# Kernel tuning notes

Hardware: AMD Instinct MI355X
Metric: run time of the kernel (lower is better)

The kernel has to match this reference:

```python
import jax, jax.numpy as jnp
import numpy as np

B, N, HID, H, DH, NB = 4, 4096, 768, 12, 64, 266
EPS = 1e-4


def softmax_kernel(data, proj, is_query):
    # data: [B,H,N,DH], proj: [NB,DH]. FAVOR+ positive softmax features.
    d = data.shape[-1]
    ratio = proj.shape[0] ** -0.5
    dn = d ** -0.25  # data normalizer
    data_dash = jnp.einsum('bhnd,jd->bhnj', data * dn, proj)  # [B,H,N,NB]
    diag = 0.5 * jnp.sum((data * dn) ** 2, axis=-1, keepdims=True)  # [B,H,N,1]
    if is_query:
        m = jnp.max(data_dash, axis=-1, keepdims=True)
    else:
        m = jnp.max(data_dash, axis=(-1, -2), keepdims=True)
    return ratio * (jnp.exp(data_dash - diag - m) + EPS)


def setup_inputs() -> dict:
    key = jax.random.key(0)
    ks = jax.random.split(key, 8)
    s = HID ** -0.5
    return {
        'hidden_states': jax.random.normal(ks[0], (B, N, HID), jnp.float32),
        'Wq': jax.random.normal(ks[1], (HID, HID), jnp.float32) * s,
        'bq': jnp.zeros((HID,), jnp.float32),
        'Wk': jax.random.normal(ks[2], (HID, HID), jnp.float32) * s,
        'bk': jnp.zeros((HID,), jnp.float32),
        'Wv': jax.random.normal(ks[3], (HID, HID), jnp.float32) * s,
        'bv': jnp.zeros((HID,), jnp.float32),
        'proj': jax.random.normal(ks[4], (NB, DH), jnp.float32),
    }


def reference(hidden_states, Wq, bq, Wk, bk, Wv, bv, proj):
    def heads(x):  # [B,N,HID] -> [B,H,N,DH]
        return x.reshape(B, N, H, DH).transpose(0, 2, 1, 3)

    q = heads(hidden_states @ Wq.T + bq)
    k = heads(hidden_states @ Wk.T + bk)
    v = heads(hidden_states @ Wv.T + bv)

    qp = softmax_kernel(q, proj, True)   # [B,H,N,NB]
    kp = softmax_kernel(k, proj, False)  # [B,H,N,NB]

    # non-causal linear attention: out = q' (k'^T v) / (q' sum_n k')
    k_sum = jnp.sum(kp, axis=2)                               # [B,H,NB]
    d_inv = 1.0 / jnp.einsum('bhnj,bhj->bhn', qp, k_sum)      # [B,H,N]
    ctx = jnp.einsum('bhnj,bhnd->bhjd', kp, v)                # [B,H,NB,DH]
    out = jnp.einsum('bhnj,bhjd->bhnd', qp, ctx) * d_inv[..., None]

    return out.transpose(0, 2, 1, 3).reshape(B, N, HID)
```

## Files before the change

kernel.cpp:

```cpp
#include <hip/hip_runtime.h>
#include <hip/hip_bf16.h>
#include <stdint.h>

#define B_   4
#define N_   4096
#define HID_ 768
#define H_   12
#define DH_  64
#define NB_  266
#define NBP_ 288
#define EPS_ 1e-4f
#define RATIO_ 0.06131393f

typedef unsigned short u16;
typedef __attribute__((ext_vector_type(8))) short short8;
typedef __attribute__((ext_vector_type(4))) float floatx4;

__device__ __forceinline__ u16 f2b(float f) {
  __hip_bfloat16 h = __float2bfloat16(f);
  return *reinterpret_cast<u16*>(&h);
}
__device__ __forceinline__ float b2f(u16 u) {
  union { unsigned u; float f; } x; x.u = ((unsigned)u) << 16; return x.f;
}
__device__ __forceinline__ unsigned fmap(float x) {
  unsigned u = __float_as_uint(x);
  return (u & 0x80000000u) ? ~u : (u | 0x80000000u);
}
__device__ __forceinline__ float funmap(unsigned u) {
  unsigned b = (u & 0x80000000u) ? (u & 0x7FFFFFFFu) : ~u;
  return __uint_as_float(b);
}
__device__ __forceinline__ void gl16(const u16* g, u16* l) {
  __builtin_amdgcn_global_load_lds(
      (const __attribute__((address_space(1))) void*)g,
      (__attribute__((address_space(3))) void*)l, 16, 0, 0);
}

__global__ __launch_bounds__(256) void k_prep(
    const float4* __restrict__ hs, const float4* __restrict__ Wq,
    const float4* __restrict__ Wk, const float4* __restrict__ Wv,
    const float* __restrict__ proj,
    uint2* __restrict__ hsb, uint2* __restrict__ wb3, u16* __restrict__ projb,
    float4* __restrict__ zf, unsigned* __restrict__ mbuf) {
  int blk = blockIdx.x;
  const int t = threadIdx.x;
  if (blk < 12288) {
    int i = blk * 256 + t;
    float4 v = hs[i];
    union { u16 s[4]; uint2 u; } pk;
    pk.s[0] = f2b(v.x); pk.s[1] = f2b(v.y); pk.s[2] = f2b(v.z); pk.s[3] = f2b(v.w);
    hsb[i] = pk.u;
    return;
  }
  blk -= 12288;
  if (blk < 1728) {
    int i = blk * 256 + t;
    int sel = i / 147456, j = i - sel * 147456;
    const float4* s = (sel == 0) ? Wq : (sel == 1) ? Wk : Wv;
    float4 v = s[j];
    union { u16 s4[4]; uint2 u; } pk;
    pk.s4[0] = f2b(v.x); pk.s4[1] = f2b(v.y); pk.s4[2] = f2b(v.z); pk.s4[3] = f2b(v.w);
    wb3[i] = pk.u;
    return;
  }
  blk -= 1728;
  if (blk < 72) {
    int i = blk * 256 + t;
    int j = i / DH_, d = i - j * DH_;
    float v = (j < NB_) ? proj[j * DH_ + d] * 0.35355339059327373f : 0.f;
    projb[i] = f2b(v);
    return;
  }
  blk -= 72;
  if (blk < 878) {
    int i = blk * 256 + t;
    if (i < 224640) zf[i] = (float4){0.f, 0.f, 0.f, 0.f};
    return;
  }
  if (t < B_ * H_) mbuf[t] = 0u;
}

__global__ __launch_bounds__(256) void k_qkv(
    const u16* __restrict__ hsb, const u16* __restrict__ wb,
    const float* __restrict__ bq, const float* __restrict__ bk, const float* __restrict__ bv,
    u16* __restrict__ qb, u16* __restrict__ kb, u16* __restrict__ vT) {
  __shared__ u16 At[2 * 128 * 32];
  __shared__ u16 Bt[2 * 128 * 32];
  const int m0 = blockIdx.x * 128;
  const int bn = blockIdx.y;
  const int sel = bn / 6;
  const int or0 = (bn % 6) * 128;
  const u16* W = wb + (size_t)sel * HID_ * HID_;
  const int t = threadIdx.x, lane = t & 63, wv = t >> 6;
  const int wr = (wv >> 1) * 64, wc = (wv & 1) * 64;
  const int lm = lane & 15, lq = lane >> 4;
  const int srow = wv * 32 + (lane >> 2);
  const int scol = (lane & 3) * 8;
  const u16* gA = hsb + (size_t)(m0 + srow) * HID_ + scol;
  const u16* gB = W + (size_t)(or0 + srow) * HID_ + scol;
  u16* lA = At + wv * 1024;
  u16* lB = Bt + wv * 1024;
  floatx4 acc[4][4];
#pragma unroll
  for (int i = 0; i < 4; i++)
#pragma unroll
    for (int j = 0; j < 4; j++) acc[i][j] = (floatx4){0.f, 0.f, 0.f, 0.f};

  for (int k0 = 0; k0 < HID_; k0 += 64) {
    __syncthreads();
#pragma unroll
    for (int p = 0; p < 2; p++) {
#pragma unroll
      for (int i = 0; i < 2; i++) {
        gl16(gA + k0 + p * 32 + i * 16 * HID_, lA + p * 4096 + i * 512);
        gl16(gB + k0 + p * 32 + i * 16 * HID_, lB + p * 4096 + i * 512);
      }
    }
    __syncthreads();
#pragma unroll
    for (int p = 0; p < 2; p++) {
      short8 af[4], bfr[4];
#pragma unroll
      for (int mt = 0; mt < 4; mt++) af[mt] = *(const short8*)&At[p * 4096 + (wr + mt * 16 + lm) * 32 + lq * 8];
#pragma unroll
      for (int nt = 0; nt < 4; nt++) bfr[nt] = *(const short8*)&Bt[p * 4096 + (wc + nt * 16 + lm) * 32 + lq * 8];
#pragma unroll
      for (int mt = 0; mt < 4; mt++)
#pragma unroll
        for (int nt = 0; nt < 4; nt++)
          acc[mt][nt] = __builtin_amdgcn_mfma_f32_16x16x32_bf16(af[mt], bfr[nt], acc[mt][nt], 0, 0, 0);
    }
  }
  if (sel < 2) {
    const float* bias = (sel == 0) ? bq : bk;
    u16* dst = (sel == 0) ? qb : kb;
#pragma unroll
    for (int mt = 0; mt < 4; mt++) {
#pragma unroll
      for (int nt = 0; nt < 4; nt++) {
        int lc = or0 + wc + nt * 16 + lm;
        float bb = bias[lc];
#pragma unroll
        for (int r = 0; r < 4; r++) {
          int row = m0 + wr + mt * 16 + lq * 4 + r;
          dst[(size_t)row * HID_ + lc] = f2b(acc[mt][nt][r] + bb);
        }
      }
    }
  } else {
#pragma unroll
    for (int mt = 0; mt < 4; mt++) {
#pragma unroll
      for (int nt = 0; nt < 4; nt++) {
        int lc = or0 + wc + nt * 16 + lm;
        int hh = lc >> 6, dv = lc & 63;
        float bb = bv[lc];
        int rowbase = m0 + wr + mt * 16 + lq * 4;
        int b = rowbase >> 12, n = rowbase & 4095;
        union { u16 s[4]; uint2 u; } pk;
#pragma unroll
        for (int r = 0; r < 4; r++) pk.s[r] = f2b(acc[mt][nt][r] + bb);
        *(uint2*)(vT + ((size_t)(b * H_ + hh) * DH_ + dv) * N_ + n) = pk.u;
      }
    }
  }
}

__global__ __launch_bounds__(256) void k_kmax2(
    const u16* __restrict__ kb, const u16* __restrict__ projb, unsigned* __restrict__ mbuf) {
  const int bh = blockIdx.y, b = bh / H_, h = bh - b * H_;
  const int n0 = blockIdx.x * 256;
  const int t = threadIdx.x, lane = t & 63, wv = t >> 6;
  const int lm = lane & 15, lq = lane >> 4;
  const u16* kbase = kb + (size_t)(b * N_ + n0 + wv * 64) * HID_ + h * DH_;
  short8 af0[4], af1[4];
#pragma unroll
  for (int mt = 0; mt < 4; mt++) {
    const u16* p = kbase + (size_t)(mt * 16 + lm) * HID_ + lq * 8;
    af0[mt] = *(const short8*)p;
    af1[mt] = *(const short8*)(p + 32);
  }
  float mx = -3e38f;
  for (int ct = 0; ct < 17; ct++) {
    const u16* pp = projb + (ct * 16 + lm) * DH_ + lq * 8;
    short8 bf0 = *(const short8*)pp;
    short8 bf1 = *(const short8*)(pp + 32);
    bool valid = (ct < 16) || (lm < 10);
#pragma unroll
    for (int mt = 0; mt < 4; mt++) {
      floatx4 a = __builtin_amdgcn_mfma_f32_16x16x32_bf16(af0[mt], bf0, (floatx4){0.f,0.f,0.f,0.f}, 0, 0, 0);
      a = __builtin_amdgcn_mfma_f32_16x16x32_bf16(af1[mt], bf1, a, 0, 0, 0);
      if (valid) {
#pragma unroll
        for (int r = 0; r < 4; r++) mx = fmaxf(mx, a[r]);
      }
    }
  }
#pragma unroll
  for (int o = 1; o < 64; o <<= 1) mx = fmaxf(mx, __shfl_xor(mx, o));
  if (lane == 0) atomicMax(&mbuf[bh], fmap(mx));
}

__global__ __launch_bounds__(256) void k_ctx3(
    const u16* __restrict__ kb, const u16* __restrict__ vT, const u16* __restrict__ projb,
    const unsigned* __restrict__ mbuf, float* __restrict__ ctxTf, float* __restrict__ ksum) {
  __shared__ u16 kpl[NBP_ * 72];
  const int bh = blockIdx.y, b = bh / H_, h = bh - b * H_;
  const int n0 = blockIdx.x * 256;
  const int t = threadIdx.x, lane = t & 63, wv = t >> 6;
  const int lm = lane & 15, lq = lane >> 4;
  const float m = funmap(mbuf[bh]);
  const u16* vTb = vT + ((size_t)bh * DH_ + wv * 16 + lm) * N_;
  floatx4 acc[18];
#pragma unroll
  for (int jt = 0; jt < 18; jt++) acc[jt] = (floatx4){0.f, 0.f, 0.f, 0.f};
  float kacc[17];
#pragma unroll
  for (int ct = 0; ct < 17; ct++) kacc[ct] = 0.f;

  for (int it = 0; it < 4; it++) {
    const int n64 = n0 + it * 64;
    __syncthreads();
    {
      const int row = n64 + wv * 16 + lm;
      const u16* kr = kb + ((size_t)(b * N_) + row) * HID_ + h * DH_ + lq * 8;
      short8 af0 = *(const short8*)kr;
      short8 af1 = *(const short8*)(kr + 32);
      float rs = 0.f;
#pragma unroll
      for (int i = 0; i < 8; i++) { float f = b2f(((const u16*)&af0)[i]); rs += f * f; }
#pragma unroll
      for (int i = 0; i < 8; i++) { float f = b2f(((const u16*)&af1)[i]); rs += f * f; }
      rs += __shfl_xor(rs, 16);
      rs += __shfl_xor(rs, 32);
      float dg[4];
#pragma unroll
      for (int r = 0; r < 4; r++) dg[r] = 0.0625f * __shfl(rs, lq * 4 + r);
#pragma unroll
      for (int ct = 0; ct < 17; ct++) {
        const u16* pp = projb + (ct * 16 + lm) * DH_ + lq * 8;
        short8 bf0 = *(const short8*)pp;
        short8 bf1 = *(const short8*)(pp + 32);
        floatx4 a = __builtin_amdgcn_mfma_f32_16x16x32_bf16(af0, bf0, (floatx4){0.f,0.f,0.f,0.f}, 0, 0, 0);
        a = __builtin_amdgcn_mfma_f32_16x16x32_bf16(af1, bf1, a, 0, 0, 0);
        bool valid = (ct < 16) || (lm < 10);
        union { u16 s[4]; uint2 u; } pk;
        float kss = 0.f;
#pragma unroll
        for (int r = 0; r < 4; r++) {
          float val = valid ? RATIO_ * (__expf(a[r] - dg[r] - m) + EPS_) : 0.f;
          kss += val;
          pk.s[r] = f2b(val);
        }
        kacc[ct] += kss;
        *(uint2*)&kpl[(ct * 16 + lm) * 72 + wv * 16 + lq * 4] = pk.u;
      }
      *(uint2*)&kpl[(272 + lm) * 72 + wv * 16 + lq * 4] = make_uint2(0u, 0u);
    }
    __syncthreads();
#pragma unroll
    for (int ns = 0; ns < 2; ns++) {
      short8 av = *(const short8*)(vTb + n64 + ns * 32 + lq * 8);
#pragma unroll
      for (int jt = 0; jt < 18; jt++) {
        short8 bf = *(const short8*)&kpl[(jt * 16 + lm) * 72 + ns * 32 + lq * 8];
        acc[jt] = __builtin_amdgcn_mfma_f32_16x16x32_bf16(av, bf, acc[jt], 0, 0, 0);
      }
    }
  }
#pragma unroll
  for (int ct = 0; ct < 17; ct++) {
    float v = kacc[ct];
    v += __shfl_xor(v, 16);
    v += __shfl_xor(v, 32);
    if (lq == 0) atomicAdd(&ksum[bh * NBP_ + ct * 16 + lm], v);
  }
#pragma unroll
  for (int jt = 0; jt < 18; jt++) {
#pragma unroll
    for (int r = 0; r < 4; r++)
      atomicAdd(&ctxTf[((size_t)bh * DH_ + wv * 16 + lq * 4 + r) * NBP_ + jt * 16 + lm], acc[jt][r]);
  }
}

__global__ void k_cvt_ctx(const float* __restrict__ src, u16* __restrict__ dst) {
  int i = blockIdx.x * 256 + threadIdx.x;
  if (i < B_ * H_ * DH_ * NBP_) dst[i] = f2b(src[i]);
}

__global__ __launch_bounds__(256) void k_out3(
    const u16* __restrict__ qb, const u16* __restrict__ projb,
    const u16* __restrict__ ctxb, const float* __restrict__ ksum,
    float* __restrict__ outp) {
  __shared__ u16 qpl[4][16][296];
  const int bh = blockIdx.y, b = bh / H_, h = bh - b * H_;
  const int n0 = blockIdx.x * 256;
  const int t = threadIdx.x, lane = t & 63, wv = t >> 6;
  const int lm = lane & 15, lq = lane >> 4;
  const u16* qbase = qb + (size_t)(b * N_ + n0 + wv * 64) * HID_ + h * DH_;
  const u16* cb = ctxb + (size_t)bh * DH_ * NBP_;
  const float* ksb = ksum + bh * NBP_;
  float ksv[17];
#pragma unroll
  for (int ct = 0; ct < 17; ct++) ksv[ct] = ksb[ct * 16 + lm];

  for (int mt = 0; mt < 4; mt++) {
    const u16* prow = qbase + (size_t)(mt * 16 + lm) * HID_ + lq * 8;
    short8 af0 = *(const short8*)prow;
    short8 af1 = *(const short8*)(prow + 32);
    float rs = 0.f;
#pragma unroll
    for (int i = 0; i < 8; i++) { float f = b2f(((const u16*)&af0)[i]); rs += f * f; }
#pragma unroll
    for (int i = 0; i < 8; i++) { float f = b2f(((const u16*)&af1)[i]); rs += f * f; }
    rs += __shfl_xor(rs, 16);
    rs += __shfl_xor(rs, 32);
    float dg[4];
#pragma unroll
    for (int r = 0; r < 4; r++) dg[r] = 0.0625f * __shfl(rs, lq * 4 + r);

    float rm[4] = {-3e38f, -3e38f, -3e38f, -3e38f};
#pragma unroll
    for (int ct = 0; ct < 17; ct++) {
      const u16* pp = projb + (ct * 16 + lm) * DH_ + lq * 8;
      short8 bf0 = *(const short8*)pp;
      short8 bf1 = *(const short8*)(pp + 32);
      floatx4 a = __builtin_amdgcn_mfma_f32_16x16x32_bf16(af0, bf0, (floatx4){0.f,0.f,0.f,0.f}, 0, 0, 0);
      a = __builtin_amdgcn_mfma_f32_16x16x32_bf16(af1, bf1, a, 0, 0, 0);
      if ((ct < 16) || (lm < 10)) {
#pragma unroll
        for (int r = 0; r < 4; r++) rm[r] = fmaxf(rm[r], a[r]);
      }
    }
#pragma unroll
    for (int o = 1; o < 16; o <<= 1) {
#pragma unroll
      for (int r = 0; r < 4; r++) rm[r] = fmaxf(rm[r], __shfl_xor(rm[r], o));
    }
    float dpart[4] = {0.f, 0.f, 0.f, 0.f};
#pragma unroll
    for (int ct = 0; ct < 18; ct++) {
      floatx4 a;
      if (ct < 17) {
        const u16* pp = projb + (ct * 16 + lm) * DH_ + lq * 8;
        short8 bf0 = *(const short8*)pp;
        short8 bf1 = *(const short8*)(pp + 32);
        a = __builtin_amdgcn_mfma_f32_16x16x32_bf16(af0, bf0, (floatx4){0.f,0.f,0.f,0.f}, 0, 0, 0);
        a = __builtin_amdgcn_mfma_f32_16x16x32_bf16(af1, bf1, a, 0, 0, 0);
      } else {
        a = (floatx4){0.f, 0.f, 0.f, 0.f};
      }
      bool valid = (ct < 16) || (ct == 16 && lm < 10);
      float kv = (ct < 17) ? ksv[ct] : 0.f;
#pragma unroll
      for (int r = 0; r < 4; r++) {
        float qpv = valid ? RATIO_ * (__expf(a[r] - dg[r] - rm[r]) + EPS_) : 0.f;
        dpart[r] += qpv * kv;
        qpl[wv][lq * 4 + r][ct * 16 + lm] = f2b(qpv);
      }
    }
#pragma unroll
    for (int o = 1; o < 16; o <<= 1) {
#pragma unroll
      for (int r = 0; r < 4; r++) dpart[r] += __shfl_xor(dpart[r], o);
    }
    float dinv[4];
#pragma unroll
    for (int r = 0; r < 4; r++) dinv[r] = 1.f / dpart[r];

    floatx4 ao[4];
#pragma unroll
    for (int dt = 0; dt < 4; dt++) ao[dt] = (floatx4){0.f, 0.f, 0.f, 0.f};
#pragma unroll
    for (int ks9 = 0; ks9 < 9; ks9++) {
      short8 aq = *(const short8*)&qpl[wv][lm][ks9 * 32 + lq * 8];
#pragma unroll
      for (int dt = 0; dt < 4; dt++) {
        short8 bc = *(const short8*)(cb + (size_t)(dt * 16 + lm) * NBP_ + ks9 * 32 + lq * 8);
        ao[dt] = __builtin_amdgcn_mfma_f32_16x16x32_bf16(aq, bc, ao[dt], 0, 0, 0);
      }
    }
#pragma unroll
    for (int dt = 0; dt < 4; dt++) {
#pragma unroll
      for (int r = 0; r < 4; r++) {
        int n = n0 + wv * 64 + mt * 16 + lq * 4 + r;
        outp[((size_t)(b * N_ + n)) * HID_ + h * DH_ + dt * 16 + lm] = ao[dt][r] * dinv[r];
      }
    }
  }
}

extern "C" void kernel_launch(void* const* d_in, const int* in_sizes, int n_in,
                              void* d_out, int out_size, void* d_ws, size_t ws_size,
                              hipStream_t stream) {
  (void)in_sizes; (void)n_in; (void)out_size; (void)ws_size;
  const float* hs   = (const float*)d_in[0];
  const float* Wq   = (const float*)d_in[1];
  const float* bq   = (const float*)d_in[2];
  const float* Wk   = (const float*)d_in[3];
  const float* bk   = (const float*)d_in[4];
  const float* Wv   = (const float*)d_in[5];
  const float* bv   = (const float*)d_in[6];
  const float* proj = (const float*)d_in[7];

  char* w = (char*)d_ws;
  u16* hsb   = (u16*)w;  w += (size_t)16384 * 768 * 2;
  u16* wb3   = (u16*)w;  w += (size_t)3 * 768 * 768 * 2;
  u16* projb = (u16*)w;  w += (size_t)NBP_ * 64 * 2;
  u16* qb    = (u16*)w;  w += (size_t)16384 * 768 * 2;
  u16* kb    = (u16*)w;  w += (size_t)16384 * 768 * 2;
  u16* vT    = (u16*)w;  w += (size_t)48 * DH_ * N_ * 2;
  float* ksum  = (float*)w; w += (size_t)48 * NBP_ * 4;
  float* ctxTf = (float*)w; w += (size_t)48 * DH_ * NBP_ * 4;
  u16* ctxTb = (u16*)w;  w += (size_t)48 * DH_ * NBP_ * 2;
  unsigned* mbuf = (unsigned*)w;

  hipLaunchKernelGGL(k_prep, dim3(14967), dim3(256), 0, stream,
                     (const float4*)hs, (const float4*)Wq, (const float4*)Wk, (const float4*)Wv,
                     proj, (uint2*)hsb, (uint2*)wb3, projb, (float4*)ksum, mbuf);
  hipLaunchKernelGGL(k_qkv, dim3(128, 18), dim3(256), 0, stream, hsb, wb3, bq, bk, bv, qb, kb, vT);
  hipLaunchKernelGGL(k_kmax2, dim3(16, 48), dim3(256), 0, stream, kb, projb, mbuf);
  hipLaunchKernelGGL(k_ctx3, dim3(16, 48), dim3(256), 0, stream, kb, vT, projb, mbuf, ctxTf, ksum);
  hipLaunchKernelGGL(k_cvt_ctx, dim3((48 * DH_ * NBP_ + 255) / 256), dim3(256), 0, stream, ctxTf, ctxTb);
  hipLaunchKernelGGL(k_out3, dim3(16, 48), dim3(256), 0, stream, qb, projb, ctxTb, ksum, (float*)d_out);
}
```

Measured before the change: 405.7 us.

## Split ctx kernel over feature columns to drop atomics, zeroing and conversion pass

The context kernel is repartitioned so each block owns 32 random-feature columns of one head and loops over all 4096 tokens, instead of owning a token chunk and atomically accumulating the full 288x64 context. Blocks now write ksum and the bf16 context directly, which removes the zero-fill in the prep kernel, the float atomics and the separate conversion kernel. The key squared norms are computed once in the max kernel and stored for reuse, and the next token tile is prefetched. In exchange, each block recomputes the key features for its column slice over the whole sequence and re-reads the keys and values 9 times. The grid shrinks to 432 longer-running blocks, with a block-index swizzle over heads.

```diff
diff --git a/kernel.cpp b/kernel.cpp
--- a/kernel.cpp
+++ b/kernel.cpp
@@ -42,7 +42,7 @@
     const float4* __restrict__ Wk, const float4* __restrict__ Wv,
     const float* __restrict__ proj,
     uint2* __restrict__ hsb, uint2* __restrict__ wb3, u16* __restrict__ projb,
-    float4* __restrict__ zf, unsigned* __restrict__ mbuf) {
+    unsigned* __restrict__ mbuf) {
   int blk = blockIdx.x;
   const int t = threadIdx.x;
   if (blk < 12288) {
@@ -73,12 +73,7 @@
     return;
   }
   blk -= 72;
-  if (blk < 878) {
-    int i = blk * 256 + t;
-    if (i < 224640) zf[i] = (float4){0.f, 0.f, 0.f, 0.f};
-    return;
-  }
-  if (t < B_ * H_) mbuf[t] = 0u;
+  if (blk == 0 && t < B_ * H_) mbuf[t] = 0u;
 }
 
 __global__ __launch_bounds__(256) void k_qkv(
@@ -167,8 +162,9 @@
   }
 }
 
-__global__ __launch_bounds__(256) void k_kmax2(
-    const u16* __restrict__ kb, const u16* __restrict__ projb, unsigned* __restrict__ mbuf) {
+__global__ __launch_bounds__(256) void k_kmax3(
+    const u16* __restrict__ kb, const u16* __restrict__ projb,
+    unsigned* __restrict__ mbuf, float* __restrict__ diagk) {
   const int bh = blockIdx.y, b = bh / H_, h = bh - b * H_;
   const int n0 = blockIdx.x * 256;
   const int t = threadIdx.x, lane = t & 63, wv = t >> 6;
@@ -181,6 +177,17 @@
     af0[mt] = *(const short8*)p;
     af1[mt] = *(const short8*)(p + 32);
   }
+#pragma unroll
+  for (int mt = 0; mt < 4; mt++) {
+    float rs = 0.f;
+#pragma unroll
+    for (int i = 0; i < 8; i++) { float f = b2f(((const u16*)&af0[mt])[i]); rs += f * f; }
+#pragma unroll
+    for (int i = 0; i < 8; i++) { float f = b2f(((const u16*)&af1[mt])[i]); rs += f * f; }
+    rs += __shfl_xor(rs, 16);
+    rs += __shfl_xor(rs, 32);
+    if (lq == 0) diagk[(size_t)bh * N_ + n0 + wv * 64 + mt * 16 + lm] = 0.0625f * rs;
+  }
   float mx = -3e38f;
   for (int ct = 0; ct < 17; ct++) {
     const u16* pp = projb + (ct * 16 + lm) * DH_ + lq * 8;
@@ -202,91 +209,107 @@
   if (lane == 0) atomicMax(&mbuf[bh], fmap(mx));
 }
 
-__global__ __launch_bounds__(256) void k_ctx3(
+__global__ __launch_bounds__(256) void k_ctx4(
     const u16* __restrict__ kb, const u16* __restrict__ vT, const u16* __restrict__ projb,
-    const unsigned* __restrict__ mbuf, float* __restrict__ ctxTf, float* __restrict__ ksum) {
-  __shared__ u16 kpl[NBP_ * 72];
-  const int bh = blockIdx.y, b = bh / H_, h = bh - b * H_;
-  const int n0 = blockIdx.x * 256;
+    const unsigned* __restrict__ mbuf, const float* __restrict__ diagk,
+    float* __restrict__ ksum, u16* __restrict__ ctxb) {
+  __shared__ u16 kpl[32 * 72];
+  __shared__ float kred[4][2][16];
+  const int orig = blockIdx.x;
+  const int lg = (orig & 7) * 54 + (orig >> 3);
+  const int bh = lg / 9, jb = lg - bh * 9;
+  const int j0 = jb * 32;
+  const int b = bh / H_, h = bh - b * H_;
   const int t = threadIdx.x, lane = t & 63, wv = t >> 6;
   const int lm = lane & 15, lq = lane >> 4;
   const float m = funmap(mbuf[bh]);
+  const bool vj0 = (j0 + lm) < NB_;
+  const bool vj1 = (j0 + 16 + lm) < NB_;
+  short8 bp00, bp01, bp10, bp11;
+  {
+    const u16* pp = projb + (j0 + lm) * DH_ + lq * 8;
+    bp00 = *(const short8*)pp;
+    bp01 = *(const short8*)(pp + 32);
+    pp += 16 * DH_;
+    bp10 = *(const short8*)pp;
+    bp11 = *(const short8*)(pp + 32);
+  }
+  const u16* kbB = kb + (size_t)(b * N_) * HID_ + h * DH_;
   const u16* vTb = vT + ((size_t)bh * DH_ + wv * 16 + lm) * N_;
-  floatx4 acc[18];
-#pragma unroll
-  for (int jt = 0; jt < 18; jt++) acc[jt] = (floatx4){0.f, 0.f, 0.f, 0.f};
-  float kacc[17];
-#pragma unroll
-  for (int ct = 0; ct < 17; ct++) kacc[ct] = 0.f;
-
-  for (int it = 0; it < 4; it++) {
-    const int n64 = n0 + it * 64;
+  const float* dgB = diagk + (size_t)bh * N_;
+  floatx4 acc0 = (floatx4){0.f,0.f,0.f,0.f}, acc1 = (floatx4){0.f,0.f,0.f,0.f};
+  float kacc0 = 0.f, kacc1 = 0.f;
+  const u16* kr0 = kbB + (size_t)(wv * 16 + lm) * HID_ + lq * 8;
+  short8 af0 = *(const short8*)kr0;
+  short8 af1 = *(const short8*)(kr0 + 32);
+  floatx4 dg4 = *(const floatx4*)(dgB + wv * 16 + lq * 4);
+
+  for (int n64 = 0; n64 < N_; n64 += 64) {
+    __syncthreads();
+    const int nn = (n64 + 64 < N_) ? n64 + 64 : 0;
+    const u16* krn = kbB + (size_t)(nn + wv * 16 + lm) * HID_ + lq * 8;
+    short8 nf0 = *(const short8*)krn;
+    short8 nf1 = *(const short8*)(krn + 32);
+    floatx4 nd = *(const floatx4*)(dgB + nn + wv * 16 + lq * 4);
+    short8 av0 = *(const short8*)(vTb + n64 + lq * 8);
+    short8 av1 = *(const short8*)(vTb + n64 + 32 + lq * 8);
+    {
+      floatx4 a = __builtin_amdgcn_mfma_f32_16x16x32_bf16(af0, bp00, (floatx4){0.f,0.f,0.f,0.f}, 0, 0, 0);
+      a = __builtin_amdgcn_mfma_f32_16x16x32_bf16(af1, bp01, a, 0, 0, 0);
+      union { u16 s[4]; uint2 u; } pk;
+      float kss = 0.f;
+#pragma unroll
+      for (int r = 0; r < 4; r++) {
+        float val = vj0 ? RATIO_ * (__expf(a[r] - dg4[r] - m) + EPS_) : 0.f;
+        kss += val;
+        pk.s[r] = f2b(val);
+      }
+      kacc0 += kss;
+      *(uint2*)&kpl[lm * 72 + wv * 16 + lq * 4] = pk.u;
+      a = __builtin_amdgcn_mfma_f32_16x16x32_bf16(af0, bp10, (floatx4){0.f,0.f,0.f,0.f}, 0, 0, 0);
+      a = __builtin_amdgcn_mfma_f32_16x16x32_bf16(af1, bp11, a, 0, 0, 0);
+      kss = 0.f;
+#pragma unroll
+      for (int r = 0; r < 4; r++) {
+        float val = vj1 ? RATIO_ * (__expf(a[r] - dg4[r] - m) + EPS_) : 0.f;
+        kss += val;
+        pk.s[r] = f2b(val);
+      }
+      kacc1 += kss;
+      *(uint2*)&kpl[(16 + lm) * 72 + wv * 16 + lq * 4] = pk.u;
+    }
     __syncthreads();
     {
-      const int row = n64 + wv * 16 + lm;
-      const u16* kr = kb + ((size_t)(b * N_) + row) * HID_ + h * DH_ + lq * 8;
-      short8 af0 = *(const short8*)kr;
-      short8 af1 = *(const short8*)(kr + 32);
-      float rs = 0.f;
-#pragma unroll
-      for (int i = 0; i < 8; i++) { float f = b2f(((const u16*)&af0)[i]); rs += f * f; }
-#pragma unroll
-      for (int i = 0; i < 8; i++) { float f = b2f(((const u16*)&af1)[i]); rs += f * f; }
-      rs += __shfl_xor(rs, 16);
-      rs += __shfl_xor(rs, 32);
-      float dg[4];
-#pragma unroll
-      for (int r = 0; r < 4; r++) dg[r] = 0.0625f * __shfl(rs, lq * 4 + r);
-#pragma unroll
-      for (int ct = 0; ct < 17; ct++) {
-        const u16* pp = projb + (ct * 16 + lm) * DH_ + lq * 8;
-        short8 bf0 = *(const short8*)pp;
-        short8 bf1 = *(const short8*)(pp + 32);
-        floatx4 a = __builtin_amdgcn_mfma_f32_16x16x32_bf16(af0, bf0, (floatx4){0.f,0.f,0.f,0.f}, 0, 0, 0);
-        a = __builtin_amdgcn_mfma_f32_16x16x32_bf16(af1, bf1, a, 0, 0, 0);
-        bool valid = (ct < 16) || (lm < 10);
-        union { u16 s[4]; uint2 u; } pk;
-        float kss = 0.f;
-#pragma unroll
-        for (int r = 0; r < 4; r++) {
-          float val = valid ? RATIO_ * (__expf(a[r] - dg[r] - m) + EPS_) : 0.f;
-          kss += val;
-          pk.s[r] = f2b(val);
-        }
-        kacc[ct] += kss;
-        *(uint2*)&kpl[(ct * 16 + lm) * 72 + wv * 16 + lq * 4] = pk.u;
-      }
-      *(uint2*)&kpl[(272 + lm) * 72 + wv * 16 + lq * 4] = make_uint2(0u, 0u);
-    }
-    __syncthreads();
-#pragma unroll
-    for (int ns = 0; ns < 2; ns++) {
-      short8 av = *(const short8*)(vTb + n64 + ns * 32 + lq * 8);
-#pragma unroll
-      for (int jt = 0; jt < 18; jt++) {
-        short8 bf = *(const short8*)&kpl[(jt * 16 + lm) * 72 + ns * 32 + lq * 8];
-        acc[jt] = __builtin_amdgcn_mfma_f32_16x16x32_bf16(av, bf, acc[jt], 0, 0, 0);
-      }
-    }
-  }
-#pragma unroll
-  for (int ct = 0; ct < 17; ct++) {
-    float v = kacc[ct];
-    v += __shfl_xor(v, 16);
-    v += __shfl_xor(v, 32);
-    if (lq == 0) atomicAdd(&ksum[bh * NBP_ + ct * 16 + lm], v);
-  }
-#pragma unroll
-  for (int jt = 0; jt < 18; jt++) {
-#pragma unroll
-    for (int r = 0; r < 4; r++)
-      atomicAdd(&ctxTf[((size_t)bh * DH_ + wv * 16 + lq * 4 + r) * NBP_ + jt * 16 + lm], acc[jt][r]);
-  }
-}
-
-__global__ void k_cvt_ctx(const float* __restrict__ src, u16* __restrict__ dst) {
-  int i = blockIdx.x * 256 + threadIdx.x;
-  if (i < B_ * H_ * DH_ * NBP_) dst[i] = f2b(src[i]);
+      short8 bf = *(const short8*)&kpl[lm * 72 + lq * 8];
+      acc0 = __builtin_amdgcn_mfma_f32_16x16x32_bf16(av0, bf, acc0, 0, 0, 0);
+      bf = *(const short8*)&kpl[(16 + lm) * 72 + lq * 8];
+      acc1 = __builtin_amdgcn_mfma_f32_16x16x32_bf16(av0, bf, acc1, 0, 0, 0);
+      bf = *(const short8*)&kpl[lm * 72 + 32 + lq * 8];
+      acc0 = __builtin_amdgcn_mfma_f32_16x16x32_bf16(av1, bf, acc0, 0, 0, 0);
+      bf = *(const short8*)&kpl[(16 + lm) * 72 + 32 + lq * 8];
+      acc1 = __builtin_amdgcn_mfma_f32_16x16x32_bf16(av1, bf, acc1, 0, 0, 0);
+    }
+    af0 = nf0; af1 = nf1; dg4 = nd;
+  }
+  {
+    float v0 = kacc0; v0 += __shfl_xor(v0, 16); v0 += __shfl_xor(v0, 32);
+    float v1 = kacc1; v1 += __shfl_xor(v1, 16); v1 += __shfl_xor(v1, 32);
+    if (lq == 0) { kred[wv][0][lm] = v0; kred[wv][1][lm] = v1; }
+  }
+  __syncthreads();
+  if (t < 32) {
+    int jh = t >> 4, l = t & 15;
+    ksum[bh * NBP_ + j0 + t] =
+        kred[0][jh][l] + kred[1][jh][l] + kred[2][jh][l] + kred[3][jh][l];
+  }
+  {
+    u16* cb = ctxb + ((size_t)bh * DH_ + wv * 16 + lq * 4) * NBP_ + j0 + lm;
+#pragma unroll
+    for (int r = 0; r < 4; r++) {
+      cb[(size_t)r * NBP_] = f2b(acc0[r]);
+      cb[(size_t)r * NBP_ + 16] = f2b(acc1[r]);
+    }
+  }
 }
 
 __global__ __launch_bounds__(256) void k_out3(
@@ -413,16 +436,15 @@
   u16* kb    = (u16*)w;  w += (size_t)16384 * 768 * 2;
   u16* vT    = (u16*)w;  w += (size_t)48 * DH_ * N_ * 2;
   float* ksum  = (float*)w; w += (size_t)48 * NBP_ * 4;
-  float* ctxTf = (float*)w; w += (size_t)48 * DH_ * NBP_ * 4;
+  float* diagk = (float*)w; w += (size_t)48 * N_ * 4;
   u16* ctxTb = (u16*)w;  w += (size_t)48 * DH_ * NBP_ * 2;
   unsigned* mbuf = (unsigned*)w;
 
-  hipLaunchKernelGGL(k_prep, dim3(14967), dim3(256), 0, stream,
+  hipLaunchKernelGGL(k_prep, dim3(14089), dim3(256), 0, stream,
                      (const float4*)hs, (const float4*)Wq, (const float4*)Wk, (const float4*)Wv,
-                     proj, (uint2*)hsb, (uint2*)wb3, projb, (float4*)ksum, mbuf);
+                     proj, (uint2*)hsb, (uint2*)wb3, projb, mbuf);
   hipLaunchKernelGGL(k_qkv, dim3(128, 18), dim3(256), 0, stream, hsb, wb3, bq, bk, bv, qb, kb, vT);
-  hipLaunchKernelGGL(k_kmax2, dim3(16, 48), dim3(256), 0, stream, kb, projb, mbuf);
-  hipLaunchKernelGGL(k_ctx3, dim3(16, 48), dim3(256), 0, stream, kb, vT, projb, mbuf, ctxTf, ksum);
-  hipLaunchKernelGGL(k_cvt_ctx, dim3((48 * DH_ * NBP_ + 255) / 256), dim3(256), 0, stream, ctxTf, ctxTb);
+  hipLaunchKernelGGL(k_kmax3, dim3(16, 48), dim3(256), 0, stream, kb, projb, mbuf, diagk);
+  hipLaunchKernelGGL(k_ctx4, dim3(432), dim3(256), 0, stream, kb, vT, projb, mbuf, diagk, ksum, ctxTb);
   hipLaunchKernelGGL(k_out3, dim3(16, 48), dim3(256), 0, stream, qb, projb, ctxTb, ksum, (float*)d_out);
 }
```

Result: faster. 365.9 us (-9.8%).
